# Kernel tuning notes

Measured on AMD Instinct MI355X. Metric: run time of the kernel, lower is better.

## Reference

```python
import jax, jax.numpy as jnp
import numpy as np
import math

C = 1024
CH = C // 2


def setup_inputs() -> dict:
    key = jax.random.key(0)
    ks = jax.random.split(key, 8)
    B, Nq, Nk = 8, 2048, 2048
    y = jax.random.normal(ks[0], (B, Nq, C), dtype=jnp.float32)
    x = jax.random.normal(ks[1], (B, Nk, C), dtype=jnp.float32)
    # torch nn.Linear weights are [out, in]; custom normal init per module
    Wq = jax.random.normal(ks[2], (CH, C), dtype=jnp.float32) * math.sqrt(2.0 / CH)
    Wk = jax.random.normal(ks[3], (CH, C), dtype=jnp.float32) * math.sqrt(2.0 / CH)
    Wv = jax.random.normal(ks[4], (C, C), dtype=jnp.float32) * math.sqrt(2.0 / C)
    # biases keep default torch Linear init: U(-1/sqrt(in), 1/sqrt(in))
    b = 1.0 / math.sqrt(C)
    bq = jax.random.uniform(ks[5], (CH,), minval=-b, maxval=b, dtype=jnp.float32)
    bk = jax.random.uniform(ks[6], (CH,), minval=-b, maxval=b, dtype=jnp.float32)
    bv = jax.random.uniform(ks[7], (C,), minval=-b, maxval=b, dtype=jnp.float32)
    return {"y": y, "x": x, "Wq": Wq, "bq": bq, "Wk": Wk, "bk": bk, "Wv": Wv, "bv": bv}


def reference(y, x, Wq, bq, Wk, bk, Wv, bv):
    scale = (C // 2) ** (-0.5)
    q = jnp.einsum('bnc,hc->bnh', y, Wq) + bq          # [B, Nq, C/2]
    k = jnp.einsum('bmc,hc->bmh', x, Wk) + bk          # [B, Nk, C/2]
    v = jnp.einsum('bmc,dc->bmd', x, Wv) + bv          # [B, Nk, C]
    dots = jnp.einsum('bnh,bmh->bnm', q, k) * scale    # [B, Nq, Nk]
    attn = jax.nn.softmax(dots, axis=-2)               # softmax over QUERY dim
    out = jnp.einsum('bnm,bmd->bnd', attn, v)          # [B, Nq, C]
    return out
```

## Files before the change

kernel.cpp:

```cpp
#include <hip/hip_runtime.h>
#include <hip/hip_bf16.h>


using bf16 = __bf16;
typedef __attribute__((ext_vector_type(8))) __bf16 bf16x8;
typedef __attribute__((ext_vector_type(4))) float f32x4;

#define GLB_AS __attribute__((address_space(1)))
#define LDS_AS __attribute__((address_space(3)))

__device__ __forceinline__ void gload_lds16(const void* g, void* l) {
  __builtin_amdgcn_global_load_lds((const GLB_AS uint32_t*)g,
                                   (LDS_AS uint32_t*)l, 16, 0, 0);
}

enum { EPI_BIAS = 0, EPI_EXP = 1, EPI_OUT = 2 };

template <int EPI>
__global__ __launch_bounds__(256) void gemm_bt(
    const bf16* __restrict__ A, const bf16* __restrict__ Bt,
    void* __restrict__ Cv, const float* __restrict__ bias,
    float* __restrict__ Z, int M, int N, int K,
    long sA, long sB, long sC, float scale) {
  __shared__ __align__(16) bf16 As[128 * 32];
  __shared__ __align__(16) bf16 Bs[128 * 32];

  const int bz = blockIdx.z;
  const bf16* Ab = A + (long)bz * sA;
  const bf16* Bb = Bt + (long)bz * sB;

  const int tid = threadIdx.x;
  const int lane = tid & 63;
  const int wave = tid >> 6;
  const long m0 = (long)blockIdx.x * 128;
  const long n0 = (long)blockIdx.y * 128;
  const int wm = (wave >> 1) * 64;
  const int wn = (wave & 1) * 64;
  const int fl = lane & 15;
  const int kg = lane >> 4;

  f32x4 acc[4][4] = {};

  const int srow = tid >> 2;
  const int scol = (tid & 3) * 8;
  const bf16* gA = Ab + (m0 + srow) * (long)K + scol;
  const bf16* gB = Bb + (n0 + srow) * (long)K + scol;
  bf16* lA = As + tid * 8;
  bf16* lB = Bs + tid * 8;

  for (int k0 = 0; k0 < K; k0 += 32) {
    __syncthreads();
    gload_lds16(gA, lA);
    gload_lds16(gA + 64L * K, lA + 2048);
    gload_lds16(gB, lB);
    gload_lds16(gB + 64L * K, lB + 2048);
    gA += 32;
    gB += 32;
    __syncthreads();

    bf16x8 a[4], b[4];
#pragma unroll
    for (int i = 0; i < 4; i++)
      a[i] = *(const bf16x8*)&As[(wm + i * 16 + fl) * 32 + kg * 8];
#pragma unroll
    for (int i = 0; i < 4; i++)
      b[i] = *(const bf16x8*)&Bs[(wn + i * 16 + fl) * 32 + kg * 8];
#pragma unroll
    for (int i = 0; i < 4; i++)
#pragma unroll
      for (int j = 0; j < 4; j++)
        acc[i][j] = __builtin_amdgcn_mfma_f32_16x16x32_bf16(a[i], b[j],
                                                            acc[i][j], 0, 0, 0);
  }

  if constexpr (EPI == EPI_BIAS) {
    bf16* Cb = (bf16*)Cv + (long)bz * sC;
#pragma unroll
    for (int j = 0; j < 4; j++) {
      const long c = n0 + wn + j * 16 + fl;
      const float bc = bias[c];
#pragma unroll
      for (int i = 0; i < 4; i++)
#pragma unroll
        for (int r = 0; r < 4; r++) {
          const long rr = m0 + wm + i * 16 + kg * 4 + r;
          Cb[rr * N + c] = (bf16)(acc[i][j][r] + bc);
        }
    }
  } else if constexpr (EPI == EPI_EXP) {
    bf16* Cb = (bf16*)Cv + (long)bz * sC;
    float* Zb = Z + (long)bz * N;
#pragma unroll
    for (int j = 0; j < 4; j++) {
      const long c = n0 + wn + j * 16 + fl;
      float s = 0.f;
#pragma unroll
      for (int i = 0; i < 4; i++)
#pragma unroll
        for (int r = 0; r < 4; r++) {
          const long rr = m0 + wm + i * 16 + kg * 4 + r;
          const float e = __expf(acc[i][j][r] * scale);
          s += e;
          Cb[rr * N + c] = (bf16)e;
        }
      atomicAdd(&Zb[c], s);
    }
  } else {
    float* Cb = (float*)Cv + (long)bz * sC;
#pragma unroll
    for (int j = 0; j < 4; j++) {
      const long c = n0 + wn + j * 16 + fl;
#pragma unroll
      for (int i = 0; i < 4; i++)
#pragma unroll
        for (int r = 0; r < 4; r++) {
          const long rr = m0 + wm + i * 16 + kg * 4 + r;
          Cb[rr * N + c] = acc[i][j][r];
        }
    }
  }
}

__global__ void cvt_f32_bf16(const float* __restrict__ in,
                             bf16* __restrict__ out, long n4) {
  long i = blockIdx.x * (long)blockDim.x + threadIdx.x;
  const long stride = (long)gridDim.x * blockDim.x;
  for (; i < n4; i += stride) {
    const float4 f = ((const float4*)in)[i];
    union { ushort4 u; bf16 h[4]; } p;
    p.h[0] = (bf16)f.x;
    p.h[1] = (bf16)f.y;
    p.h[2] = (bf16)f.z;
    p.h[3] = (bf16)f.w;
    ((ushort4*)out)[i] = p.u;
  }
}

__global__ __launch_bounds__(256) void transpose_scale(
    const bf16* __restrict__ v, const float* __restrict__ Z,
    bf16* __restrict__ vt) {
  __shared__ bf16 tile[32][33];
  const int b = blockIdx.z;
  const bf16* vb = v + (long)b * 2048 * 1024;
  bf16* vtb = vt + (long)b * 1024 * 2048;
  const float* Zb = Z + b * 2048;
  const int m0 = blockIdx.x * 32, d0 = blockIdx.y * 32;
  const int t = threadIdx.x;
  const int r = t >> 3, c4 = (t & 7) * 4;

  union { ushort4 u; bf16 h[4]; } in;
  in.u = *(const ushort4*)&vb[(long)(m0 + r) * 1024 + d0 + c4];
  tile[r][c4 + 0] = in.h[0];
  tile[r][c4 + 1] = in.h[1];
  tile[r][c4 + 2] = in.h[2];
  tile[r][c4 + 3] = in.h[3];
  __syncthreads();

  union { ushort4 u; bf16 h[4]; } o;
#pragma unroll
  for (int j = 0; j < 4; j++) {
    const float val = (float)tile[c4 + j][r] / Zb[m0 + c4 + j];
    o.h[j] = (bf16)val;
  }
  *(ushort4*)&vtb[(long)(d0 + r) * 2048 + m0 + c4] = o.u;
}

extern "C" void kernel_launch(void* const* d_in, const int* in_sizes, int n_in,
                              void* d_out, int out_size, void* d_ws,
                              size_t ws_size, hipStream_t stream) {
  const float* y = (const float*)d_in[0];
  const float* x = (const float*)d_in[1];
  const float* Wq = (const float*)d_in[2];
  const float* bq = (const float*)d_in[3];
  const float* Wk = (const float*)d_in[4];
  const float* bk = (const float*)d_in[5];
  const float* Wv = (const float*)d_in[6];
  const float* bv = (const float*)d_in[7];
  float* out = (float*)d_out;

  constexpr long B = 8, Nq = 2048, Nk = 2048, Cd = 1024, CH = 512;
  constexpr long BNq = B * Nq;
  const float scale = 0.04419417382415922f;

  char* w = (char*)d_ws;
  auto alloc = [&](size_t bytes) {
    char* p = w;
    w += (bytes + 255) & ~(size_t)255;
    return p;
  };
  bf16* y_bf = (bf16*)alloc(BNq * Cd * 2);
  bf16* x_bf = (bf16*)alloc(BNq * Cd * 2);
  bf16* Wq_bf = (bf16*)alloc(CH * Cd * 2);
  bf16* Wk_bf = (bf16*)alloc(CH * Cd * 2);
  bf16* Wv_bf = (bf16*)alloc(Cd * Cd * 2);
  bf16* q_bf = (bf16*)alloc(BNq * CH * 2);
  bf16* k_bf = (bf16*)alloc(BNq * CH * 2);
  bf16* v_bf = (bf16*)alloc(BNq * Cd * 2);
  bf16* vt_bf = (bf16*)alloc(BNq * Cd * 2);
  bf16* P_bf = (bf16*)alloc(B * Nq * Nk * 2);
  float* Zsum = (float*)alloc(B * Nk * 4);
  if ((size_t)(w - (char*)d_ws) > ws_size) return;

  cvt_f32_bf16<<<2048, 256, 0, stream>>>(y, y_bf, BNq * Cd / 4);
  cvt_f32_bf16<<<2048, 256, 0, stream>>>(x, x_bf, BNq * Cd / 4);
  cvt_f32_bf16<<<512, 256, 0, stream>>>(Wq, Wq_bf, CH * Cd / 4);
  cvt_f32_bf16<<<512, 256, 0, stream>>>(Wk, Wk_bf, CH * Cd / 4);
  cvt_f32_bf16<<<1024, 256, 0, stream>>>(Wv, Wv_bf, Cd * Cd / 4);

  gemm_bt<EPI_BIAS><<<dim3(128, 4, 1), 256, 0, stream>>>(
      y_bf, Wq_bf, q_bf, bq, nullptr, BNq, CH, Cd, 0, 0, 0, 0.f);
  gemm_bt<EPI_BIAS><<<dim3(128, 4, 1), 256, 0, stream>>>(
      x_bf, Wk_bf, k_bf, bk, nullptr, BNq, CH, Cd, 0, 0, 0, 0.f);
  gemm_bt<EPI_BIAS><<<dim3(128, 8, 1), 256, 0, stream>>>(
      x_bf, Wv_bf, v_bf, bv, nullptr, BNq, Cd, Cd, 0, 0, 0, 0.f);

  hipMemsetAsync(Zsum, 0, B * Nk * 4, stream);
  gemm_bt<EPI_EXP><<<dim3(16, 16, 8), 256, 0, stream>>>(
      q_bf, k_bf, P_bf, nullptr, Zsum, Nq, Nk, CH,
      Nq * CH, Nk * CH, Nq * Nk, scale);

  transpose_scale<<<dim3(64, 32, 8), 256, 0, stream>>>(v_bf, Zsum, vt_bf);

  gemm_bt<EPI_OUT><<<dim3(16, 8, 8), 256, 0, stream>>>(
      P_bf, vt_bf, out, nullptr, nullptr, Nq, Cd, Nk,
      Nq * Nk, Cd * Nk, Nq * Cd, 0.f);
}
```

Measured before the change: 527.5 us.

## Use 256x256 multi-stage pipelined GEMM and fuse K/V projections

Replaces the 128x128 single-buffered GEMM with a 256x256 tile, 512-thread kernel. It keeps a four-buffer LDS ring filled by async global-to-LDS loads three k-steps ahead, paced with explicit vmcnt/lgkmcnt waits, barriers and setprio around the MFMA bursts. The K and V projections are merged into one GEMM over a concatenated weight and bias, so x is read once. Downstream kernels now read K and V through strided leading dimensions. The goal is more data reuse per tile, hidden load latency and fewer launches. The cost is 128 KB of LDS per block, which allows only one block per CU, more register pressure, and a vmcnt(8) wait in the last iterations that may not cover the final outstanding stages.

```diff
diff --git a/kernel.cpp b/kernel.cpp
--- a/kernel.cpp
+++ b/kernel.cpp
@@ -14,16 +14,20 @@
                                    (LDS_AS uint32_t*)l, 16, 0, 0);
 }
 
+#define BAR() __builtin_amdgcn_s_barrier()
+#define LGK0() asm volatile("s_waitcnt lgkmcnt(0)" ::: "memory")
+#define VM8() asm volatile("s_waitcnt vmcnt(8)" ::: "memory")
+
 enum { EPI_BIAS = 0, EPI_EXP = 1, EPI_OUT = 2 };
 
 template <int EPI>
-__global__ __launch_bounds__(256) void gemm_bt(
+__global__ __launch_bounds__(512, 2) void gemm256(
     const bf16* __restrict__ A, const bf16* __restrict__ Bt,
     void* __restrict__ Cv, const float* __restrict__ bias,
-    float* __restrict__ Z, int M, int N, int K,
+    float* __restrict__ Z, int M, int N, int K, int ldA, int ldB, int ldC,
     long sA, long sB, long sC, float scale) {
-  __shared__ __align__(16) bf16 As[128 * 32];
-  __shared__ __align__(16) bf16 Bs[128 * 32];
+  __shared__ __align__(16) bf16 As[4 * 8192];
+  __shared__ __align__(16) bf16 Bs[4 * 8192];
 
   const int bz = blockIdx.z;
   const bf16* Ab = A + (long)bz * sA;
@@ -32,59 +36,102 @@
   const int tid = threadIdx.x;
   const int lane = tid & 63;
   const int wave = tid >> 6;
-  const long m0 = (long)blockIdx.x * 128;
-  const long n0 = (long)blockIdx.y * 128;
-  const int wm = (wave >> 1) * 64;
-  const int wn = (wave & 1) * 64;
+  const int wr = wave >> 2;
+  const int wc = wave & 3;
   const int fl = lane & 15;
   const int kg = lane >> 4;
-
-  f32x4 acc[4][4] = {};
+  const long m0 = (long)blockIdx.x * 256;
+  const long n0 = (long)blockIdx.y * 256;
+
+  f32x4 acc[8][4] = {};
 
   const int srow = tid >> 2;
   const int scol = (tid & 3) * 8;
-  const bf16* gA = Ab + (m0 + srow) * (long)K + scol;
-  const bf16* gB = Bb + (n0 + srow) * (long)K + scol;
-  bf16* lA = As + tid * 8;
-  bf16* lB = Bs + tid * 8;
-
-  for (int k0 = 0; k0 < K; k0 += 32) {
-    __syncthreads();
-    gload_lds16(gA, lA);
-    gload_lds16(gA + 64L * K, lA + 2048);
-    gload_lds16(gB, lB);
-    gload_lds16(gB + 64L * K, lB + 2048);
-    gA += 32;
-    gB += 32;
-    __syncthreads();
-
-    bf16x8 a[4], b[4];
-#pragma unroll
-    for (int i = 0; i < 4; i++)
-      a[i] = *(const bf16x8*)&As[(wm + i * 16 + fl) * 32 + kg * 8];
-#pragma unroll
-    for (int i = 0; i < 4; i++)
-      b[i] = *(const bf16x8*)&Bs[(wn + i * 16 + fl) * 32 + kg * 8];
-#pragma unroll
-    for (int i = 0; i < 4; i++)
-#pragma unroll
-      for (int j = 0; j < 4; j++)
-        acc[i][j] = __builtin_amdgcn_mfma_f32_16x16x32_bf16(a[i], b[j],
-                                                            acc[i][j], 0, 0, 0);
-  }
+  const bf16* gA0 = Ab + (m0 + srow) * (long)ldA + scol;
+  const bf16* gA1 = Ab + (m0 + 128 + srow) * (long)ldA + scol;
+  const bf16* gB0 = Bb + (n0 + srow) * (long)ldB + scol;
+  const bf16* gB1 = Bb + (n0 + 128 + srow) * (long)ldB + scol;
+  const int l0 = tid * 8, l1 = 4096 + tid * 8;
+
+  const int nt = K >> 5;
+
+#define STAGE_A(tt)                                    \
+  {                                                    \
+    const int _b = ((tt) & 3) * 8192;                  \
+    const long _k = (long)(tt) * 32;                   \
+    gload_lds16(gA0 + _k, &As[_b + l0]);               \
+    gload_lds16(gA1 + _k, &As[_b + l1]);               \
+  }
+#define STAGE_B(tt)                                    \
+  {                                                    \
+    const int _b = ((tt) & 3) * 8192;                  \
+    const long _k = (long)(tt) * 32;                   \
+    gload_lds16(gB0 + _k, &Bs[_b + l0]);               \
+    gload_lds16(gB1 + _k, &Bs[_b + l1]);               \
+  }
+#define RD_A(bo, i, mh) \
+  (*(const bf16x8*)&As[(bo) + (wr * 128 + (mh)*64 + (i)*16 + fl) * 32 + kg * 8])
+#define RD_B(bo, j) \
+  (*(const bf16x8*)&Bs[(bo) + (wc * 64 + (j)*16 + fl) * 32 + kg * 8])
+
+  STAGE_A(0) STAGE_B(0) STAGE_A(1) STAGE_B(1) STAGE_A(2) STAGE_B(2)
+  VM8();
+  BAR();
+
+  for (int t = 0; t < nt; ++t) {
+    const int bo = (t & 3) * 8192;
+    const int tt = t + 3;
+    bf16x8 a0, a1, a2, a3, b0, b1, b2, b3;
+    a0 = RD_A(bo, 0, 0); a1 = RD_A(bo, 1, 0);
+    a2 = RD_A(bo, 2, 0); a3 = RD_A(bo, 3, 0);
+    b0 = RD_B(bo, 0); b1 = RD_B(bo, 1); b2 = RD_B(bo, 2); b3 = RD_B(bo, 3);
+    if (tt < nt) STAGE_A(tt);
+    BAR();
+    LGK0();
+    __builtin_amdgcn_s_setprio(1);
+#pragma unroll
+    for (int j = 0; j < 4; j++) {
+      acc[0][j] = __builtin_amdgcn_mfma_f32_16x16x32_bf16(a0, j == 0 ? b0 : j == 1 ? b1 : j == 2 ? b2 : b3, acc[0][j], 0, 0, 0);
+      acc[1][j] = __builtin_amdgcn_mfma_f32_16x16x32_bf16(a1, j == 0 ? b0 : j == 1 ? b1 : j == 2 ? b2 : b3, acc[1][j], 0, 0, 0);
+      acc[2][j] = __builtin_amdgcn_mfma_f32_16x16x32_bf16(a2, j == 0 ? b0 : j == 1 ? b1 : j == 2 ? b2 : b3, acc[2][j], 0, 0, 0);
+      acc[3][j] = __builtin_amdgcn_mfma_f32_16x16x32_bf16(a3, j == 0 ? b0 : j == 1 ? b1 : j == 2 ? b2 : b3, acc[3][j], 0, 0, 0);
+    }
+    __builtin_amdgcn_s_setprio(0);
+    BAR();
+    a0 = RD_A(bo, 0, 1); a1 = RD_A(bo, 1, 1);
+    a2 = RD_A(bo, 2, 1); a3 = RD_A(bo, 3, 1);
+    if (tt < nt) STAGE_B(tt);
+    BAR();
+    LGK0();
+    __builtin_amdgcn_s_setprio(1);
+#pragma unroll
+    for (int j = 0; j < 4; j++) {
+      acc[4][j] = __builtin_amdgcn_mfma_f32_16x16x32_bf16(a0, j == 0 ? b0 : j == 1 ? b1 : j == 2 ? b2 : b3, acc[4][j], 0, 0, 0);
+      acc[5][j] = __builtin_amdgcn_mfma_f32_16x16x32_bf16(a1, j == 0 ? b0 : j == 1 ? b1 : j == 2 ? b2 : b3, acc[5][j], 0, 0, 0);
+      acc[6][j] = __builtin_amdgcn_mfma_f32_16x16x32_bf16(a2, j == 0 ? b0 : j == 1 ? b1 : j == 2 ? b2 : b3, acc[6][j], 0, 0, 0);
+      acc[7][j] = __builtin_amdgcn_mfma_f32_16x16x32_bf16(a3, j == 0 ? b0 : j == 1 ? b1 : j == 2 ? b2 : b3, acc[7][j], 0, 0, 0);
+    }
+    __builtin_amdgcn_s_setprio(0);
+    VM8();
+    BAR();
+  }
+#undef STAGE_A
+#undef STAGE_B
+#undef RD_A
+#undef RD_B
 
   if constexpr (EPI == EPI_BIAS) {
     bf16* Cb = (bf16*)Cv + (long)bz * sC;
 #pragma unroll
     for (int j = 0; j < 4; j++) {
-      const long c = n0 + wn + j * 16 + fl;
-      const float bc = bias[c];
-#pragma unroll
-      for (int i = 0; i < 4; i++)
-#pragma unroll
-        for (int r = 0; r < 4; r++) {
-          const long rr = m0 + wm + i * 16 + kg * 4 + r;
-          Cb[rr * N + c] = (bf16)(acc[i][j][r] + bc);
+      const long cc = n0 + wc * 64 + j * 16 + fl;
+      const float bc = bias[cc];
+#pragma unroll
+      for (int mi = 0; mi < 8; mi++)
+#pragma unroll
+        for (int e = 0; e < 4; e++) {
+          const long rr = m0 + wr * 128 + mi * 16 + kg * 4 + e;
+          Cb[rr * ldC + cc] = (bf16)(acc[mi][j][e] + bc);
         }
     }
   } else if constexpr (EPI == EPI_EXP) {
@@ -92,30 +139,30 @@
     float* Zb = Z + (long)bz * N;
 #pragma unroll
     for (int j = 0; j < 4; j++) {
-      const long c = n0 + wn + j * 16 + fl;
-      float s = 0.f;
-#pragma unroll
-      for (int i = 0; i < 4; i++)
-#pragma unroll
-        for (int r = 0; r < 4; r++) {
-          const long rr = m0 + wm + i * 16 + kg * 4 + r;
-          const float e = __expf(acc[i][j][r] * scale);
-          s += e;
-          Cb[rr * N + c] = (bf16)e;
+      const long cc = n0 + wc * 64 + j * 16 + fl;
+      float zp = 0.f;
+#pragma unroll
+      for (int mi = 0; mi < 8; mi++)
+#pragma unroll
+        for (int e = 0; e < 4; e++) {
+          const long rr = m0 + wr * 128 + mi * 16 + kg * 4 + e;
+          const float ex = __expf(acc[mi][j][e] * scale);
+          zp += ex;
+          Cb[rr * ldC + cc] = (bf16)ex;
         }
-      atomicAdd(&Zb[c], s);
+      atomicAdd(&Zb[cc], zp);
     }
   } else {
     float* Cb = (float*)Cv + (long)bz * sC;
 #pragma unroll
     for (int j = 0; j < 4; j++) {
-      const long c = n0 + wn + j * 16 + fl;
-#pragma unroll
-      for (int i = 0; i < 4; i++)
-#pragma unroll
-        for (int r = 0; r < 4; r++) {
-          const long rr = m0 + wm + i * 16 + kg * 4 + r;
-          Cb[rr * N + c] = acc[i][j][r];
+      const long cc = n0 + wc * 64 + j * 16 + fl;
+#pragma unroll
+      for (int mi = 0; mi < 8; mi++)
+#pragma unroll
+        for (int e = 0; e < 4; e++) {
+          const long rr = m0 + wr * 128 + mi * 16 + kg * 4 + e;
+          Cb[rr * ldC + cc] = acc[mi][j][e];
         }
     }
   }
@@ -137,11 +184,11 @@
 }
 
 __global__ __launch_bounds__(256) void transpose_scale(
-    const bf16* __restrict__ v, const float* __restrict__ Z,
+    const bf16* __restrict__ kv, const float* __restrict__ Z,
     bf16* __restrict__ vt) {
   __shared__ bf16 tile[32][33];
   const int b = blockIdx.z;
-  const bf16* vb = v + (long)b * 2048 * 1024;
+  const bf16* vb = kv + (long)b * 2048 * 1536 + 512;
   bf16* vtb = vt + (long)b * 1024 * 2048;
   const float* Zb = Z + b * 2048;
   const int m0 = blockIdx.x * 32, d0 = blockIdx.y * 32;
@@ -149,7 +196,7 @@
   const int r = t >> 3, c4 = (t & 7) * 4;
 
   union { ushort4 u; bf16 h[4]; } in;
-  in.u = *(const ushort4*)&vb[(long)(m0 + r) * 1024 + d0 + c4];
+  in.u = *(const ushort4*)&vb[(long)(m0 + r) * 1536 + d0 + c4];
   tile[r][c4 + 0] = in.h[0];
   tile[r][c4 + 1] = in.h[1];
   tile[r][c4 + 2] = in.h[2];
@@ -158,10 +205,8 @@
 
   union { ushort4 u; bf16 h[4]; } o;
 #pragma unroll
-  for (int j = 0; j < 4; j++) {
-    const float val = (float)tile[c4 + j][r] / Zb[m0 + c4 + j];
-    o.h[j] = (bf16)val;
-  }
+  for (int j = 0; j < 4; j++)
+    o.h[j] = (bf16)((float)tile[c4 + j][r] / Zb[m0 + c4 + j]);
   *(ushort4*)&vtb[(long)(d0 + r) * 2048 + m0 + c4] = o.u;
 }
 
@@ -179,7 +224,7 @@
   float* out = (float*)d_out;
 
   constexpr long B = 8, Nq = 2048, Nk = 2048, Cd = 1024, CH = 512;
-  constexpr long BNq = B * Nq;
+  constexpr long BN = B * Nq;
   const float scale = 0.04419417382415922f;
 
   char* w = (char*)d_ws;
@@ -188,40 +233,40 @@
     w += (bytes + 255) & ~(size_t)255;
     return p;
   };
-  bf16* y_bf = (bf16*)alloc(BNq * Cd * 2);
-  bf16* x_bf = (bf16*)alloc(BNq * Cd * 2);
+  bf16* y_bf = (bf16*)alloc(BN * Cd * 2);
+  bf16* x_bf = (bf16*)alloc(BN * Cd * 2);
   bf16* Wq_bf = (bf16*)alloc(CH * Cd * 2);
-  bf16* Wk_bf = (bf16*)alloc(CH * Cd * 2);
-  bf16* Wv_bf = (bf16*)alloc(Cd * Cd * 2);
-  bf16* q_bf = (bf16*)alloc(BNq * CH * 2);
-  bf16* k_bf = (bf16*)alloc(BNq * CH * 2);
-  bf16* v_bf = (bf16*)alloc(BNq * Cd * 2);
-  bf16* vt_bf = (bf16*)alloc(BNq * Cd * 2);
+  bf16* Wkv_bf = (bf16*)alloc((CH + Cd) * Cd * 2);
+  float* bkv = (float*)alloc((CH + Cd) * 4);
+  bf16* q_bf = (bf16*)alloc(BN * CH * 2);
+  bf16* kv_bf = (bf16*)alloc(BN * (CH + Cd) * 2);
+  bf16* vt_bf = (bf16*)alloc(BN * Cd * 2);
   bf16* P_bf = (bf16*)alloc(B * Nq * Nk * 2);
   float* Zsum = (float*)alloc(B * Nk * 4);
   if ((size_t)(w - (char*)d_ws) > ws_size) return;
 
-  cvt_f32_bf16<<<2048, 256, 0, stream>>>(y, y_bf, BNq * Cd / 4);
-  cvt_f32_bf16<<<2048, 256, 0, stream>>>(x, x_bf, BNq * Cd / 4);
+  cvt_f32_bf16<<<2048, 256, 0, stream>>>(y, y_bf, BN * Cd / 4);
+  cvt_f32_bf16<<<2048, 256, 0, stream>>>(x, x_bf, BN * Cd / 4);
   cvt_f32_bf16<<<512, 256, 0, stream>>>(Wq, Wq_bf, CH * Cd / 4);
-  cvt_f32_bf16<<<512, 256, 0, stream>>>(Wk, Wk_bf, CH * Cd / 4);
-  cvt_f32_bf16<<<1024, 256, 0, stream>>>(Wv, Wv_bf, Cd * Cd / 4);
-
-  gemm_bt<EPI_BIAS><<<dim3(128, 4, 1), 256, 0, stream>>>(
-      y_bf, Wq_bf, q_bf, bq, nullptr, BNq, CH, Cd, 0, 0, 0, 0.f);
-  gemm_bt<EPI_BIAS><<<dim3(128, 4, 1), 256, 0, stream>>>(
-      x_bf, Wk_bf, k_bf, bk, nullptr, BNq, CH, Cd, 0, 0, 0, 0.f);
-  gemm_bt<EPI_BIAS><<<dim3(128, 8, 1), 256, 0, stream>>>(
-      x_bf, Wv_bf, v_bf, bv, nullptr, BNq, Cd, Cd, 0, 0, 0, 0.f);
+  cvt_f32_bf16<<<512, 256, 0, stream>>>(Wk, Wkv_bf, CH * Cd / 4);
+  cvt_f32_bf16<<<1024, 256, 0, stream>>>(Wv, Wkv_bf + CH * Cd, Cd * Cd / 4);
+  hipMemcpyAsync(bkv, bk, CH * 4, hipMemcpyDeviceToDevice, stream);
+  hipMemcpyAsync(bkv + CH, bv, Cd * 4, hipMemcpyDeviceToDevice, stream);
+
+  gemm256<EPI_BIAS><<<dim3(64, 2, 1), 512, 0, stream>>>(
+      y_bf, Wq_bf, q_bf, bq, nullptr, BN, CH, Cd, Cd, Cd, CH, 0, 0, 0, 0.f);
+  gemm256<EPI_BIAS><<<dim3(64, 6, 1), 512, 0, stream>>>(
+      x_bf, Wkv_bf, kv_bf, bkv, nullptr, BN, CH + Cd, Cd, Cd, Cd, CH + Cd,
+      0, 0, 0, 0.f);
 
   hipMemsetAsync(Zsum, 0, B * Nk * 4, stream);
-  gemm_bt<EPI_EXP><<<dim3(16, 16, 8), 256, 0, stream>>>(
-      q_bf, k_bf, P_bf, nullptr, Zsum, Nq, Nk, CH,
-      Nq * CH, Nk * CH, Nq * Nk, scale);
-
-  transpose_scale<<<dim3(64, 32, 8), 256, 0, stream>>>(v_bf, Zsum, vt_bf);
-
-  gemm_bt<EPI_OUT><<<dim3(16, 8, 8), 256, 0, stream>>>(
-      P_bf, vt_bf, out, nullptr, nullptr, Nq, Cd, Nk,
+  gemm256<EPI_EXP><<<dim3(8, 8, 8), 512, 0, stream>>>(
+      q_bf, kv_bf, P_bf, nullptr, Zsum, Nq, Nk, CH, CH, CH + Cd, Nk,
+      Nq * CH, Nk * (CH + Cd), Nq * Nk, scale);
+
+  transpose_scale<<<dim3(64, 32, 8), 256, 0, stream>>>(kv_bf, Zsum, vt_bf);
+
+  gemm256<EPI_OUT><<<dim3(8, 4, 8), 512, 0, stream>>>(
+      P_bf, vt_bf, out, nullptr, nullptr, Nq, Cd, Nk, Nk, Nk, Cd,
       Nq * Nk, Cd * Nk, Nq * Cd, 0.f);
 }
```

Result: faster. 479.0 us (-9.2%).
